# Optimization experiments

Measured on AMD Instinct MI355X. Metric: run time of the kernel, lower is better.

## Reference

```python
import jax, jax.numpy as jnp
import numpy as np

H = 8      # n_heads
HD = 64    # per-head channels (out_channels in __init__, before *= n_heads)


def setup_inputs() -> dict:
    key = jax.random.key(0)
    ks = jax.random.split(key, 10)
    B, C, N = 4, 256, 2048
    O = H * HD
    s = 1.0 / np.sqrt(C).astype(np.float32)
    return {
        "x": jax.random.normal(ks[0], (B, C, N), dtype=jnp.float32),
        "y": jax.random.normal(ks[1], (B, C, N), dtype=jnp.float32),
        "Wq": jax.random.normal(ks[2], (O, C), dtype=jnp.float32) * s,
        "bq": jnp.zeros((O,), dtype=jnp.float32),
        "Wk": jax.random.normal(ks[3], (O, C), dtype=jnp.float32) * s,
        "bk": jnp.zeros((O,), dtype=jnp.float32),
        "Wv": jax.random.normal(ks[4], (O, C), dtype=jnp.float32) * s,
        "bv": jnp.zeros((O,), dtype=jnp.float32),
        "Wp": jax.random.normal(ks[5], (HD, C), dtype=jnp.float32) * s,  # residual projection, bias=False
        "gamma": jax.random.uniform(ks[6], (H, 1, 1, 1), dtype=jnp.float32) + 0.001,
    }


def _conv1x1(W, b, t):
    # 1x1 Conv1d: (O,C) x (B,C,N) -> (B,O,N)
    out = jnp.einsum('oc,bcn->bon', W, t)
    return out if b is None else out + b[None, :, None]


def _heads(t):
    # (B, H*HD, N) -> (H, B, N, HD); channel split into contiguous per-head chunks
    B, _, N = t.shape
    return t.reshape(B, H, HD, N).transpose(1, 0, 3, 2)


def reference(x, y, Wq, bq, Wk, bk, Wv, bv, Wp, gamma):
    # q/k/v projections via 1x1 convs (kernel_size=1, 'stride_effective' padding => same length)
    q = _heads(_conv1x1(Wq, bq, x))   # (H,B,N,HD)
    k = _heads(_conv1x1(Wk, bk, y))   # (H,B,N,HD)
    v = _heads(_conv1x1(Wv, bv, y))   # (H,B,N,HD)

    # energy = bmm(Q, K^T); softmax over last dim (no mask)
    energy = jnp.einsum('hbnd,hbmd->hbnm', q, k)          # (H,B,N,N)
    attn = jax.nn.softmax(energy, axis=-1)

    # out = bmm(attention.transpose(-2,-1), V)  (note the transpose in the original)
    out = jnp.einsum('hbnm,hbnd->hbmd', attn, v)          # (H,B,N,HD)

    # gamma-weighted residual blend with projected y
    yp = _conv1x1(Wp, None, y).transpose(0, 2, 1)         # (B,N,HD)
    g = gamma.reshape(H, 1, 1, 1)
    out = (g * out + yp[None]) / (1.0 + g)                # (H,B,N,HD)
    return out
```

## Files before the change

### kernel.cpp

```cpp
#include <hip/hip_runtime.h>
#include <math.h>
#include <stdint.h>

#define B_DIM 4
#define C_DIM 256
#define N_DIM 2048
#define H_DIM 8
#define HD    64
#define HB    32
#define NTOK  (B_DIM * N_DIM)
#define LOG2E 1.44269504f

typedef __attribute__((ext_vector_type(8))) short bf16x8;
typedef __attribute__((ext_vector_type(4))) float f32x4;
typedef __attribute__((ext_vector_type(16))) float f32x16;
typedef __attribute__((ext_vector_type(4))) unsigned u32x4;

static __device__ __forceinline__ short f2bf(float f) {
    unsigned u = __builtin_bit_cast(unsigned, f);
    u += 0x7fffu + ((u >> 16) & 1u);
    return (short)(u >> 16);
}
static __device__ __forceinline__ float bf2f(short s) {
    unsigned u = ((unsigned)(unsigned short)s) << 16;
    return __builtin_bit_cast(float, u);
}
static __device__ __forceinline__ float fx2(float x) {
#if __has_builtin(__builtin_amdgcn_exp2f)
    return __builtin_amdgcn_exp2f(x);
#else
    return exp2f(x);
#endif
}
static __device__ __forceinline__ unsigned pk_bf16(float a, float b) {
#if __has_builtin(__builtin_amdgcn_cvt_pk_bf16_f32)
    auto v = __builtin_amdgcn_cvt_pk_bf16_f32(a, b);
    return __builtin_bit_cast(unsigned, v);
#else
    unsigned ua = __builtin_bit_cast(unsigned, a);
    unsigned ub = __builtin_bit_cast(unsigned, b);
    return ((ua + 0x8000u) >> 16) | ((ub + 0x8000u) & 0xffff0000u);
#endif
}
static __device__ __forceinline__ void pl32swap(unsigned &a, unsigned &b) {
#if __has_builtin(__builtin_amdgcn_permlane32_swap)
    typedef __attribute__((ext_vector_type(2))) int i32x2_t;
    i32x2_t r = __builtin_amdgcn_permlane32_swap((int)a, (int)b, false, false);
    a = (unsigned)r[0]; b = (unsigned)r[1];
#else
    unsigned sa = __shfl_xor(a, 32), sb = __shfl_xor(b, 32);
    bool hi = (threadIdx.x & 32) != 0;
    unsigned na = hi ? sb : a;
    unsigned nb = hi ? b : sa;
    a = na; b = nb;
#endif
}

static __device__ __forceinline__ void gll16(const void* g, void* ldsbase, int lane) {
#if __has_builtin(__builtin_amdgcn_global_load_lds)
    __builtin_amdgcn_global_load_lds(
        (const __attribute__((address_space(1))) void*)(uintptr_t)(g),
        (__attribute__((address_space(3))) void*)(uintptr_t)(ldsbase), 16, 0, 0);
#else
    *(bf16x8*)((char*)ldsbase + lane * 16) = *(const bf16x8*)g;
#endif
}

#define MFMA16(A, Bv, Cv) __builtin_amdgcn_mfma_f32_16x16x32_bf16(A, Bv, Cv, 0, 0, 0)
#define MFMA32(A, Bv, Cv) __builtin_amdgcn_mfma_f32_32x32x16_bf16(A, Bv, Cv, 0, 0, 0)


__global__ __launch_bounds__(256) void cast_all(
    const float* __restrict__ X, const float* __restrict__ Y,
    const float* __restrict__ Wq, const float* __restrict__ Wk,
    const float* __restrict__ Wv, const float* __restrict__ Wp,
    short* __restrict__ XS, short* __restrict__ YS,
    short* __restrict__ WSx, short* __restrict__ WSy)
{
    const int z = blockIdx.z;
    const int t = threadIdx.x;

    if (z == 8) {
        int base = (blockIdx.y * 32 + blockIdx.x) * 256 + t;
#pragma unroll
        for (int rep = 0; rep < 2; ++rep) {
            int gid = base + rep * 32768;
            if (gid >= 51200) break;
            int lane = gid & 63, chunk = gid >> 6;
            int lo = lane & 15, quad = lane >> 4;
            const float* src; short* dst;
            if (chunk < 256) {
                int ot = chunk >> 3, ks = chunk & 7;
                src = Wq + (size_t)(ot * 16 + lo) * C_DIM + ks * 32 + quad * 8;
                dst = WSx + (size_t)chunk * 512 + lane * 8;
            } else {
                int ch = chunk - 256;
                int ot = ch >> 3, ks = ch & 7;
                int row = ot * 16 + lo;
                const float* basep = (row < 512) ? (Wk + (size_t)row * C_DIM)
                                   : (row < 1024) ? (Wv + (size_t)(row - 512) * C_DIM)
                                                  : (Wp + (size_t)(row - 1024) * C_DIM);
                src = basep + ks * 32 + quad * 8;
                dst = WSy + (size_t)ch * 512 + lane * 8;
            }
            bf16x8 o;
#pragma unroll
            for (int j = 0; j < 8; ++j) o[j] = f2bf(src[j]);
            *(bf16x8*)dst = o;
        }
        return;
    }

    const float* src = (z < 4) ? X : Y;
    short* dst = (z < 4) ? XS : YS;
    const int b = z & 3, c0 = blockIdx.y * 64, n0 = blockIdx.x * 64;
    __shared__ float L[64][65];
    for (int i = t; i < 4096; i += 256) {
        int cc = i >> 6, nn = i & 63;
        L[cc][nn] = src[((size_t)b * C_DIM + c0 + cc) * N_DIM + n0 + nn];
    }
    __syncthreads();
#pragma unroll
    for (int half = 0; half < 2; ++half) {
        int cid = half * 256 + t;
        int lane = cid & 63, fi = cid >> 6;
        int ksl = fi & 1, rtl = fi >> 1;
        int lo = lane & 15, quad = lane >> 4;
        bf16x8 o;
#pragma unroll
        for (int j = 0; j < 8; ++j) o[j] = f2bf(L[ksl * 32 + quad * 8 + j][rtl * 16 + lo]);
        int rt = b * 128 + (n0 >> 4) + rtl;
        int ks = (c0 >> 5) + ksl;
        *(bf16x8*)(dst + ((size_t)(rt * 8 + ks) * 64 + lane) * 8) = o;
    }
}

__global__ __launch_bounds__(256) void proj_all(
    const short* __restrict__ WSx, const short* __restrict__ WSy,
    const short* __restrict__ XS, const short* __restrict__ YS,
    const float* __restrict__ bq, const float* __restrict__ bk,
    const float* __restrict__ bv,
    short* __restrict__ QS, short* __restrict__ KS,
    short* __restrict__ VSu, float* __restrict__ Yo)
{
    const int oy = blockIdx.y;
    const bool isq = oy < 8;
    const short* WS = isq ? WSx : WSy;
    const short* Xs = isq ? XS : YS;
    const int oyl = isq ? oy : oy - 8;
    const int o0 = oyl * 64;
    const int tok0 = blockIdx.x * 128;
    const int t = threadIdx.x, wave = t >> 6, lane = t & 63;
    const int lo = lane & 15, quad = lane >> 4;

    __shared__ __align__(16) char smem[34816];

    const int ot = oyl * 4 + wave;
    const int rt0 = tok0 >> 4;
    const f32x4 czero = {0.f, 0.f, 0.f, 0.f};

    f32x4 acc[8];
#pragma unroll
    for (int i = 0; i < 8; ++i) acc[i] = czero;

#pragma unroll 2
    for (int ks = 0; ks < 8; ++ks) {
        bf16x8 a = *(const bf16x8*)(WS + ((size_t)(ot * 8 + ks) * 64 + lane) * 8);
#pragma unroll
        for (int nt = 0; nt < 8; ++nt) {
            bf16x8 bx = *(const bf16x8*)(Xs + ((size_t)((rt0 + nt) * 8 + ks) * 64 + lane) * 8);
            acc[nt] = MFMA16(a, bx, acc[nt]);
        }
    }

    const int b = tok0 >> 11;
    const int n0b = tok0 & (N_DIM - 1);

    if (oy < 16) {
        short* T = (short*)smem;
        const float* bias = isq ? bq : bk;
        const float scale = isq ? LOG2E : 1.f;
        float bvr[4];
#pragma unroll
        for (int r = 0; r < 4; ++r) bvr[r] = bias[o0 + wave * 16 + quad * 4 + r];
#pragma unroll
        for (int nt = 0; nt < 8; ++nt) {
            short4 pk;
            pk.x = f2bf((acc[nt][0] + bvr[0]) * scale);
            pk.y = f2bf((acc[nt][1] + bvr[1]) * scale);
            pk.z = f2bf((acc[nt][2] + bvr[2]) * scale);
            pk.w = f2bf((acc[nt][3] + bvr[3]) * scale);
            *(short4*)(T + (nt * 16 + lo) * 72 + wave * 16 + quad * 4) = pk;
        }
        __syncthreads();
        const int h = oyl;
        const int hb = h * 4 + b;
        short* dst = isq ? QS : KS;
#pragma unroll
        for (int s = 0; s < 4; ++s) {
            int cid = s * 256 + t;
            int ln = cid & 63, fi = cid >> 6;
            int ks = fi & 3, nt2l = fi >> 2;
            bf16x8 v = *(const bf16x8*)(T + (nt2l * 32 + (ln & 31)) * 72
                                          + ks * 16 + ((ln >> 5) << 3));
            size_t frag = ((size_t)(hb * 64) + (n0b >> 5) + nt2l) * 4 + ks;
            *(bf16x8*)(dst + frag * 512 + ln * 8) = v;
        }
    } else if (oy < 24) {
        short* T2 = (short*)smem;
        float bvr[4];
#pragma unroll
        for (int r = 0; r < 4; ++r) bvr[r] = bv[o0 - 512 + wave * 16 + quad * 4 + r];
#pragma unroll
        for (int nt = 0; nt < 8; ++nt)
#pragma unroll
            for (int r = 0; r < 4; ++r) {
                int ol = wave * 16 + quad * 4 + r;
                T2[ol * 136 + nt * 16 + lo] = f2bf(acc[nt][r] + bvr[r]);
            }
        __syncthreads();
        const int h = oy - 16;
        const int hb = h * 4 + b;
#pragma unroll
        for (int s = 0; s < 4; ++s) {
            int cid = s * 256 + t;
            int ln = cid & 63, fi = cid >> 6;
            int dt2 = fi & 1, nk = (fi >> 1) & 3, nbl = fi >> 3;
            bf16x8 v = *(const bf16x8*)(T2 + (dt2 * 32 + (ln & 31)) * 136
                                           + nbl * 64 + nk * 16 + ((ln >> 5) << 3));
            size_t frag = (((size_t)(hb * 32) + (n0b >> 6) + nbl) * 4 + nk) * 2 + dt2;
            *(bf16x8*)(VSu + frag * 512 + ln * 8) = v;
        }
    } else {
        float* T3 = (float*)smem;
#pragma unroll
        for (int nt = 0; nt < 8; ++nt) {
            float4 f;
            f.x = acc[nt][0]; f.y = acc[nt][1]; f.z = acc[nt][2]; f.w = acc[nt][3];
            *(float4*)(T3 + (nt * 16 + lo) * 68 + wave * 16 + quad * 4) = f;
        }
        __syncthreads();
#pragma unroll
        for (int s = 0; s < 8; ++s) {
            int cid = s * 256 + t;
            int row = cid >> 4, c4 = (cid & 15) * 4;
            float4 f = *(const float4*)(T3 + row * 68 + c4);
            *(float4*)(Yo + ((size_t)(tok0 + row)) * 64 + c4) = f;
        }
    }
}

__global__ __launch_bounds__(256, 4) void rowsum_mfma(
    const short* __restrict__ QS, const short* __restrict__ KS,
    float* __restrict__ RSp, float* __restrict__ RSpW)
{
    const int id = blockIdx.x;
    const int hb = ((id & 7) << 2) | ((id >> 3) & 3);
    const int zq = (id >> 5) & 3;
    const int n0 = (id >> 7) * 256;
    const int t = threadIdx.x, wave = t >> 6, lane = t & 63;
    const int hi = lane >> 5;
    f32x16 czero16;
#pragma unroll
    for (int r = 0; r < 16; ++r) czero16[r] = 0.f;

    bf16x8 qf[2][4];
    const short* qb = QS + ((size_t)(hb * 64 + (n0 >> 5) + wave * 2)) * 4 * 512 + lane * 8;
#pragma unroll
    for (int tt = 0; tt < 2; ++tt)
#pragma unroll
        for (int ks = 0; ks < 4; ++ks)
            qf[tt][ks] = *(const bf16x8*)(qb + (tt * 4 + ks) * 512);

    float sm[2][16];
#pragma unroll
    for (int tt = 0; tt < 2; ++tt)
#pragma unroll
        for (int r = 0; r < 16; ++r) sm[tt][r] = 0.f;

    const short* kp = KS + ((size_t)(hb * 64 + zq * 16)) * 4 * 512 + lane * 8;
    for (int mt = 0; mt < 16; ++mt) {
        bf16x8 kf[4];
#pragma unroll
        for (int ks = 0; ks < 4; ++ks)
            kf[ks] = *(const bf16x8*)(kp + (mt * 4 + ks) * 512);
#pragma unroll
        for (int tt = 0; tt < 2; ++tt) {
            f32x16 cc = czero16;
#pragma unroll
            for (int ks = 0; ks < 4; ++ks) cc = MFMA32(qf[tt][ks], kf[ks], cc);
#pragma unroll
            for (int r = 0; r < 16; ++r) sm[tt][r] += fx2(cc[r]);
        }
    }

#pragma unroll
    for (int sft = 1; sft < 32; sft <<= 1)
#pragma unroll
        for (int tt = 0; tt < 2; ++tt)
#pragma unroll
            for (int r = 0; r < 16; ++r) sm[tt][r] += __shfl_xor(sm[tt][r], sft);

    if ((lane & 31) == 0) {
        float* dst = (zq < 2) ? (RSp  + (size_t)zq * HB * N_DIM)
                              : (RSpW + (size_t)(zq - 2) * HB * N_DIM);
#pragma unroll
        for (int tt = 0; tt < 2; ++tt)
#pragma unroll
            for (int g = 0; g < 4; ++g) {
                int n = n0 + wave * 64 + tt * 32 + g * 8 + hi * 4;
                float4 v = {sm[tt][g * 4 + 0], sm[tt][g * 4 + 1],
                            sm[tt][g * 4 + 2], sm[tt][g * 4 + 3]};
                *(float4*)(dst + (size_t)hb * N_DIM + n) = v;
            }
    }
}

__global__ __launch_bounds__(256) void v_scale(
    const short* __restrict__ VSu, const float* __restrict__ RSp,
    const float* __restrict__ RSpW, short* __restrict__ VS)
{
    int t = blockIdx.x * 256 + threadIdx.x;
    int lane = t & 63, fidx = t >> 6;
    int dt2 = fidx & 1; (void)dt2;
    int nk = (fidx >> 1) & 3, nb = (fidx >> 3) & 31, hb = fidx >> 8;
    int n = nb * 64 + nk * 16 + ((lane >> 5) << 3);
    bf16x8 v = *(const bf16x8*)(VSu + (size_t)t * 8);
    const float* r0 = RSp  + (size_t)hb * N_DIM + n;
    const float* r1 = r0 + (size_t)HB * N_DIM;
    const float* r2 = RSpW + (size_t)hb * N_DIM + n;
    const float* r3 = r2 + (size_t)HB * N_DIM;
    bf16x8 o;
#pragma unroll
    for (int j = 0; j < 8; ++j)
        o[j] = f2bf(bf2f(v[j]) / ((r0[j] + r1[j]) + (r2[j] + r3[j])));
    *(bf16x8*)(VS + (size_t)t * 8) = o;
}

__global__ __launch_bounds__(256, 3) void attnout_mfma(
    const short* __restrict__ QS, const short* __restrict__ KS,
    const short* __restrict__ VS,
    short* __restrict__ PA0, short* __restrict__ PA1)
{
    const int id = blockIdx.x;
    const int hb = ((id & 7) << 2) | ((id >> 3) & 3);
    const int z = (id >> 5) & 1;
    const int m0 = (id >> 6) * 128;

    __shared__ __align__(16) char smem[34816];
    char* Qst = smem;
    char* Vst = smem + 16384;

    const int t = threadIdx.x, wave = t >> 6, lane = t & 63;
    const f32x4 cz4 = {0.f, 0.f, 0.f, 0.f}; (void)cz4;
    f32x16 czero16;
#pragma unroll
    for (int r = 0; r < 16; ++r) czero16[r] = 0.f;

    bf16x8 kf[4];
    {
        const short* kbase = KS + ((size_t)(hb * 64 + (m0 >> 5) + wave)) * 4 * 512 + lane * 8;
#pragma unroll
        for (int ks = 0; ks < 4; ++ks)
            kf[ks] = *(const bf16x8*)(kbase + ks * 512);
    }

    f32x16 oacc[2];
#pragma unroll
    for (int dt2 = 0; dt2 < 2; ++dt2) oacc[dt2] = czero16;

    const short* qsrc = QS + ((size_t)(hb * 64 + z * 32)) * 4 * 512 + lane * 8;
    const short* vsrc = VS + ((size_t)(hb * 32 + z * 16)) * 8 * 512 + lane * 8;
    const int NIT = N_DIM / 2 / 64;

    f32x16 c[2];
    bf16x8 pa[4];

    gll16(qsrc + (size_t)wave * 512,            Qst + wave * 1024, lane);
    gll16(qsrc + (size_t)(wave + 4) * 512,      Qst + (wave + 4) * 1024, lane);
    gll16(qsrc + (size_t)(8 + wave) * 512,      Qst + 8192 + wave * 1024, lane);
    gll16(qsrc + (size_t)(8 + wave + 4) * 512,  Qst + 8192 + (wave + 4) * 1024, lane);
    gll16(vsrc + (size_t)wave * 512,            Vst + wave * 1024, lane);
    gll16(vsrc + (size_t)(wave + 4) * 512,      Vst + (wave + 4) * 1024, lane);
    __syncthreads();
#pragma unroll
    for (int tt = 0; tt < 2; ++tt) {
        f32x16 cc = czero16;
#pragma unroll
        for (int ks = 0; ks < 4; ++ks) {
            bf16x8 a = *(const bf16x8*)(Qst + (tt * 4 + ks) * 1024 + lane * 16);
            cc = MFMA32(a, kf[ks], cc);
        }
        c[tt] = cc;
    }
    __syncthreads();

    for (int i = 0; i < NIT - 1; ++i) {
        gll16(qsrc + ((size_t)(i + 2) * 8 + wave) * 512,
              Qst + (i & 1) * 8192 + wave * 1024, lane);
        gll16(qsrc + ((size_t)(i + 2) * 8 + wave + 4) * 512,
              Qst + (i & 1) * 8192 + (wave + 4) * 1024, lane);
        gll16(vsrc + ((size_t)(i + 1) * 8 + wave) * 512,
              Vst + ((i + 1) & 1) * 8192 + wave * 1024, lane);
        gll16(vsrc + ((size_t)(i + 1) * 8 + wave + 4) * 512,
              Vst + ((i + 1) & 1) * 8192 + (wave + 4) * 1024, lane);
#pragma unroll
        for (int tt = 0; tt < 2; ++tt) {
#pragma unroll
            for (int half = 0; half < 2; ++half) {
                unsigned w01 = pk_bf16(fx2(c[tt][half * 8 + 0]), fx2(c[tt][half * 8 + 1]));
                unsigned w23 = pk_bf16(fx2(c[tt][half * 8 + 2]), fx2(c[tt][half * 8 + 3]));
                unsigned w45 = pk_bf16(fx2(c[tt][half * 8 + 4]), fx2(c[tt][half * 8 + 5]));
                unsigned w67 = pk_bf16(fx2(c[tt][half * 8 + 6]), fx2(c[tt][half * 8 + 7]));
                pl32swap(w01, w45);
                pl32swap(w23, w67);
                u32x4 f = {w01, w23, w45, w67};
                pa[tt * 2 + half] = __builtin_bit_cast(bf16x8, f);
            }
        }
        {
            const char* Qb = Qst + ((i + 1) & 1) * 8192;
            __builtin_amdgcn_s_setprio(1);
#pragma unroll
            for (int tt = 0; tt < 2; ++tt) {
                f32x16 cc = czero16;
#pragma unroll
                for (int ks = 0; ks < 4; ++ks) {
                    bf16x8 a = *(const bf16x8*)(Qb + (tt * 4 + ks) * 1024 + lane * 16);
                    cc = MFMA32(a, kf[ks], cc);
                }
                c[tt] = cc;
            }
            __builtin_amdgcn_s_setprio(0);
        }
        {
            const char* vb = Vst + (i & 1) * 8192;
#pragma unroll
            for (int nk = 0; nk < 4; ++nk)
#pragma unroll
                for (int dt2 = 0; dt2 < 2; ++dt2) {
                    bf16x8 bv = *(const bf16x8*)(vb + (nk * 2 + dt2) * 1024 + lane * 16);
                    oacc[dt2] = MFMA32(pa[nk], bv, oacc[dt2]);
                }
        }
        __syncthreads();
    }

#pragma unroll
    for (int tt = 0; tt < 2; ++tt) {
#pragma unroll
        for (int half = 0; half < 2; ++half) {
            unsigned w01 = pk_bf16(fx2(c[tt][half * 8 + 0]), fx2(c[tt][half * 8 + 1]));
            unsigned w23 = pk_bf16(fx2(c[tt][half * 8 + 2]), fx2(c[tt][half * 8 + 3]));
            unsigned w45 = pk_bf16(fx2(c[tt][half * 8 + 4]), fx2(c[tt][half * 8 + 5]));
            unsigned w67 = pk_bf16(fx2(c[tt][half * 8 + 6]), fx2(c[tt][half * 8 + 7]));
            pl32swap(w01, w45);
            pl32swap(w23, w67);
            u32x4 f = {w01, w23, w45, w67};
            pa[tt * 2 + half] = __builtin_bit_cast(bf16x8, f);
        }
    }
    {
        const char* vb = Vst + ((NIT - 1) & 1) * 8192;
#pragma unroll
        for (int nk = 0; nk < 4; ++nk)
#pragma unroll
            for (int dt2 = 0; dt2 < 2; ++dt2) {
                bf16x8 bv = *(const bf16x8*)(vb + (nk * 2 + dt2) * 1024 + lane * 16);
                oacc[dt2] = MFMA32(pa[nk], bv, oacc[dt2]);
            }
    }

    short* PA = z ? PA1 : PA0;
    float* T = (float*)smem;
    const int hi = lane >> 5;
    __syncthreads();
#pragma unroll
    for (int dt2 = 0; dt2 < 2; ++dt2)
#pragma unroll
        for (int r = 0; r < 16; ++r) {
            int row = wave * 32 + (r & 3) + 8 * (r >> 2) + 4 * hi;
            T[row * 68 + dt2 * 32 + (lane & 31)] = oacc[dt2][r];
        }
    __syncthreads();
#pragma unroll
    for (int it = 0; it < 4; ++it) {
        int idx = it * 256 + t;
        int rowl = idx >> 3, dg = (idx & 7) * 8;
        float4 f0 = *(const float4*)(T + rowl * 68 + dg);
        float4 f1 = *(const float4*)(T + rowl * 68 + dg + 4);
        uint4 o;
        o.x = pk_bf16(f0.x, f0.y);
        o.y = pk_bf16(f0.z, f0.w);
        o.z = pk_bf16(f1.x, f1.y);
        o.w = pk_bf16(f1.z, f1.w);
        int m = m0 + rowl;
        *(uint4*)(PA + ((size_t)(hb * N_DIM + m)) * 64 + dg) = o;
    }
}

__global__ __launch_bounds__(256) void combine_out(
    const short* __restrict__ PA0, const short* __restrict__ PA1,
    const float* __restrict__ YP, const float* __restrict__ gamma,
    float* __restrict__ out)
{
    size_t flat = ((size_t)blockIdx.x * 256 + threadIdx.x) * 8;
    int d  = (int)(flat & 63);
    int n  = (int)((flat >> 6) & (N_DIM - 1));
    int hb = (int)(flat >> 17);
    int h = hb >> 2, b = hb & 3;
    float g = gamma[h];
    float inv = 1.f / (1.f + g);
    float gi = g * inv;
    bf16x8 p0 = *(const bf16x8*)(PA0 + flat);
    bf16x8 p1 = *(const bf16x8*)(PA1 + flat);
    const float* yp = YP + ((size_t)b * N_DIM + n) * HD + d;
    float o[8];
#pragma unroll
    for (int j = 0; j < 8; ++j)
        o[j] = gi * (bf2f(p0[j]) + bf2f(p1[j])) + inv * yp[j];
    float4 o0 = {o[0], o[1], o[2], o[3]};
    float4 o1 = {o[4], o[5], o[6], o[7]};
    *(float4*)(out + flat) = o0;
    *(float4*)(out + flat + 4) = o1;
}

extern "C" void kernel_launch(void* const* d_in, const int* in_sizes, int n_in,
                              void* d_out, int out_size, void* d_ws, size_t ws_size,
                              hipStream_t stream) {
    const float* x     = (const float*)d_in[0];
    const float* y     = (const float*)d_in[1];
    const float* Wq    = (const float*)d_in[2];
    const float* bq    = (const float*)d_in[3];
    const float* Wk    = (const float*)d_in[4];
    const float* bk    = (const float*)d_in[5];
    const float* Wv    = (const float*)d_in[6];
    const float* bv    = (const float*)d_in[7];
    const float* Wp    = (const float*)d_in[8];
    const float* gamma = (const float*)d_in[9];
    float* out = (float*)d_out;

    const size_t XEL  = (size_t)B_DIM * C_DIM * N_DIM;
    const size_t QKV  = (size_t)HB * N_DIM * HD;

    short* XS  = (short*)d_ws;
    short* YS  = XS + XEL;
    short* WSx = YS + XEL;
    short* WSy = WSx + 512 * C_DIM;
    short* QS  = WSy + 1088 * C_DIM;
    short* KS  = QS + QKV;
    short* VSu = KS + QKV;
    short* VS  = VSu + QKV;
    float* YPb = (float*)(VS + QKV);
    float* RSp = YPb + (size_t)B_DIM * N_DIM * HD;
    short* PA0 = XS;
    short* PA1 = VSu;
    float* RSpW = (float*)WSx;

    dim3 blk(256);
    cast_all<<<dim3(N_DIM / 64, C_DIM / 64, 9), blk, 0, stream>>>(
        x, y, Wq, Wk, Wv, Wp, XS, YS, WSx, WSy);

    proj_all<<<dim3(NTOK / 128, 25), blk, 0, stream>>>(
        WSx, WSy, XS, YS, bq, bk, bv, QS, KS, VSu, YPb);

    rowsum_mfma<<<dim3(1024), blk, 0, stream>>>(QS, KS, RSp, RSpW);
    v_scale<<<dim3(2048), blk, 0, stream>>>(VSu, RSp, RSpW, VS);
    attnout_mfma<<<dim3(1024), blk, 0, stream>>>(QS, KS, VS, PA0, PA1);
    combine_out<<<dim3(2048), blk, 0, stream>>>(PA0, PA1, YPb, gamma, out);
}
```

Baseline: 191.9 us.

## Process two m-tiles per block in attnout to reuse staged Q and V

Each attnout block now covers 256 output rows instead of 128. Every wave holds two sets of K fragments and two output accumulators, so each Q and V tile staged in shared memory feeds twice as many MFMAs. This halves the block count and the global and LDS traffic for Q and V per unit of work. In exchange, register pressure rises, launch bounds drop to 2 blocks per CU, and the grid shrinks to 512 blocks, which may hurt latency hiding or leave CUs underfilled.

```diff
diff --git a/kernel.cpp b/kernel.cpp
--- a/kernel.cpp
+++ b/kernel.cpp
@@ -337,7 +337,7 @@
     *(bf16x8*)(VS + (size_t)t * 8) = o;
 }
 
-__global__ __launch_bounds__(256, 3) void attnout_mfma(
+__global__ __launch_bounds__(256, 2) void attnout_mfma(
     const short* __restrict__ QS, const short* __restrict__ KS,
     const short* __restrict__ VS,
     short* __restrict__ PA0, short* __restrict__ PA1)
@@ -345,36 +345,39 @@
     const int id = blockIdx.x;
     const int hb = ((id & 7) << 2) | ((id >> 3) & 3);
     const int z = (id >> 5) & 1;
-    const int m0 = (id >> 6) * 128;
+    const int m0 = (id >> 6) * 256;
 
     __shared__ __align__(16) char smem[34816];
     char* Qst = smem;
     char* Vst = smem + 16384;
 
     const int t = threadIdx.x, wave = t >> 6, lane = t & 63;
-    const f32x4 cz4 = {0.f, 0.f, 0.f, 0.f}; (void)cz4;
     f32x16 czero16;
 #pragma unroll
     for (int r = 0; r < 16; ++r) czero16[r] = 0.f;
 
-    bf16x8 kf[4];
-    {
-        const short* kbase = KS + ((size_t)(hb * 64 + (m0 >> 5) + wave)) * 4 * 512 + lane * 8;
+    bf16x8 kf[2][4];
+#pragma unroll
+    for (int mm = 0; mm < 2; ++mm) {
+        const short* kbase = KS + ((size_t)(hb * 64 + (m0 >> 5) + mm * 4 + wave)) * 4 * 512
+                           + lane * 8;
 #pragma unroll
         for (int ks = 0; ks < 4; ++ks)
-            kf[ks] = *(const bf16x8*)(kbase + ks * 512);
-    }
-
-    f32x16 oacc[2];
-#pragma unroll
-    for (int dt2 = 0; dt2 < 2; ++dt2) oacc[dt2] = czero16;
+            kf[mm][ks] = *(const bf16x8*)(kbase + ks * 512);
+    }
+
+    f32x16 oacc[2][2];
+#pragma unroll
+    for (int mm = 0; mm < 2; ++mm)
+#pragma unroll
+        for (int dt2 = 0; dt2 < 2; ++dt2) oacc[mm][dt2] = czero16;
 
     const short* qsrc = QS + ((size_t)(hb * 64 + z * 32)) * 4 * 512 + lane * 8;
     const short* vsrc = VS + ((size_t)(hb * 32 + z * 16)) * 8 * 512 + lane * 8;
     const int NIT = N_DIM / 2 / 64;
 
-    f32x16 c[2];
-    bf16x8 pa[4];
+    f32x16 c[2][2];
+    bf16x8 pa[2][4];
 
     gll16(qsrc + (size_t)wave * 512,            Qst + wave * 1024, lane);
     gll16(qsrc + (size_t)(wave + 4) * 512,      Qst + (wave + 4) * 1024, lane);
@@ -385,13 +388,14 @@
     __syncthreads();
 #pragma unroll
     for (int tt = 0; tt < 2; ++tt) {
-        f32x16 cc = czero16;
+        f32x16 c0 = czero16, c1 = czero16;
 #pragma unroll
         for (int ks = 0; ks < 4; ++ks) {
             bf16x8 a = *(const bf16x8*)(Qst + (tt * 4 + ks) * 1024 + lane * 16);
-            cc = MFMA32(a, kf[ks], cc);
-        }
-        c[tt] = cc;
+            c0 = MFMA32(a, kf[0][ks], c0);
+            c1 = MFMA32(a, kf[1][ks], c1);
+        }
+        c[tt][0] = c0; c[tt][1] = c1;
     }
     __syncthreads();
 
@@ -405,61 +409,65 @@
         gll16(vsrc + ((size_t)(i + 1) * 8 + wave + 4) * 512,
               Vst + ((i + 1) & 1) * 8192 + (wave + 4) * 1024, lane);
 #pragma unroll
-        for (int tt = 0; tt < 2; ++tt) {
+        for (int mm = 0; mm < 2; ++mm)
+#pragma unroll
+            for (int tt = 0; tt < 2; ++tt)
+#pragma unroll
+                for (int half = 0; half < 2; ++half) {
+                    unsigned w01 = pk_bf16(fx2(c[tt][mm][half * 8 + 0]), fx2(c[tt][mm][half * 8 + 1]));
+                    unsigned w23 = pk_bf16(fx2(c[tt][mm][half * 8 + 2]), fx2(c[tt][mm][half * 8 + 3]));
+                    unsigned w45 = pk_bf16(fx2(c[tt][mm][half * 8 + 4]), fx2(c[tt][mm][half * 8 + 5]));
+                    unsigned w67 = pk_bf16(fx2(c[tt][mm][half * 8 + 6]), fx2(c[tt][mm][half * 8 + 7]));
+                    pl32swap(w01, w45);
+                    pl32swap(w23, w67);
+                    u32x4 f = {w01, w23, w45, w67};
+                    pa[mm][tt * 2 + half] = __builtin_bit_cast(bf16x8, f);
+                }
+        {
+            const char* Qb = Qst + ((i + 1) & 1) * 8192;
+            __builtin_amdgcn_s_setprio(1);
+#pragma unroll
+            for (int tt = 0; tt < 2; ++tt) {
+                f32x16 c0 = czero16, c1 = czero16;
+#pragma unroll
+                for (int ks = 0; ks < 4; ++ks) {
+                    bf16x8 a = *(const bf16x8*)(Qb + (tt * 4 + ks) * 1024 + lane * 16);
+                    c0 = MFMA32(a, kf[0][ks], c0);
+                    c1 = MFMA32(a, kf[1][ks], c1);
+                }
+                c[tt][0] = c0; c[tt][1] = c1;
+            }
+            __builtin_amdgcn_s_setprio(0);
+        }
+        {
+            const char* vb = Vst + (i & 1) * 8192;
+#pragma unroll
+            for (int nk = 0; nk < 4; ++nk)
+#pragma unroll
+                for (int dt2 = 0; dt2 < 2; ++dt2) {
+                    bf16x8 bv = *(const bf16x8*)(vb + (nk * 2 + dt2) * 1024 + lane * 16);
+                    oacc[0][dt2] = MFMA32(pa[0][nk], bv, oacc[0][dt2]);
+                    oacc[1][dt2] = MFMA32(pa[1][nk], bv, oacc[1][dt2]);
+                }
+        }
+        __syncthreads();
+    }
+
+#pragma unroll
+    for (int mm = 0; mm < 2; ++mm)
+#pragma unroll
+        for (int tt = 0; tt < 2; ++tt)
 #pragma unroll
             for (int half = 0; half < 2; ++half) {
-                unsigned w01 = pk_bf16(fx2(c[tt][half * 8 + 0]), fx2(c[tt][half * 8 + 1]));
-                unsigned w23 = pk_bf16(fx2(c[tt][half * 8 + 2]), fx2(c[tt][half * 8 + 3]));
-                unsigned w45 = pk_bf16(fx2(c[tt][half * 8 + 4]), fx2(c[tt][half * 8 + 5]));
-                unsigned w67 = pk_bf16(fx2(c[tt][half * 8 + 6]), fx2(c[tt][half * 8 + 7]));
+                unsigned w01 = pk_bf16(fx2(c[tt][mm][half * 8 + 0]), fx2(c[tt][mm][half * 8 + 1]));
+                unsigned w23 = pk_bf16(fx2(c[tt][mm][half * 8 + 2]), fx2(c[tt][mm][half * 8 + 3]));
+                unsigned w45 = pk_bf16(fx2(c[tt][mm][half * 8 + 4]), fx2(c[tt][mm][half * 8 + 5]));
+                unsigned w67 = pk_bf16(fx2(c[tt][mm][half * 8 + 6]), fx2(c[tt][mm][half * 8 + 7]));
                 pl32swap(w01, w45);
                 pl32swap(w23, w67);
                 u32x4 f = {w01, w23, w45, w67};
-                pa[tt * 2 + half] = __builtin_bit_cast(bf16x8, f);
-            }
-        }
-        {
-            const char* Qb = Qst + ((i + 1) & 1) * 8192;
-            __builtin_amdgcn_s_setprio(1);
-#pragma unroll
-            for (int tt = 0; tt < 2; ++tt) {
-                f32x16 cc = czero16;
-#pragma unroll
-                for (int ks = 0; ks < 4; ++ks) {
-                    bf16x8 a = *(const bf16x8*)(Qb + (tt * 4 + ks) * 1024 + lane * 16);
-                    cc = MFMA32(a, kf[ks], cc);
-                }
-                c[tt] = cc;
-            }
-            __builtin_amdgcn_s_setprio(0);
-        }
-        {
-            const char* vb = Vst + (i & 1) * 8192;
-#pragma unroll
-            for (int nk = 0; nk < 4; ++nk)
-#pragma unroll
-                for (int dt2 = 0; dt2 < 2; ++dt2) {
-                    bf16x8 bv = *(const bf16x8*)(vb + (nk * 2 + dt2) * 1024 + lane * 16);
-                    oacc[dt2] = MFMA32(pa[nk], bv, oacc[dt2]);
-                }
-        }
-        __syncthreads();
-    }
-
-#pragma unroll
-    for (int tt = 0; tt < 2; ++tt) {
-#pragma unroll
-        for (int half = 0; half < 2; ++half) {
-            unsigned w01 = pk_bf16(fx2(c[tt][half * 8 + 0]), fx2(c[tt][half * 8 + 1]));
-            unsigned w23 = pk_bf16(fx2(c[tt][half * 8 + 2]), fx2(c[tt][half * 8 + 3]));
-            unsigned w45 = pk_bf16(fx2(c[tt][half * 8 + 4]), fx2(c[tt][half * 8 + 5]));
-            unsigned w67 = pk_bf16(fx2(c[tt][half * 8 + 6]), fx2(c[tt][half * 8 + 7]));
-            pl32swap(w01, w45);
-            pl32swap(w23, w67);
-            u32x4 f = {w01, w23, w45, w67};
-            pa[tt * 2 + half] = __builtin_bit_cast(bf16x8, f);
-        }
-    }
+                pa[mm][tt * 2 + half] = __builtin_bit_cast(bf16x8, f);
+            }
     {
         const char* vb = Vst + ((NIT - 1) & 1) * 8192;
 #pragma unroll
@@ -467,35 +475,39 @@
 #pragma unroll
             for (int dt2 = 0; dt2 < 2; ++dt2) {
                 bf16x8 bv = *(const bf16x8*)(vb + (nk * 2 + dt2) * 1024 + lane * 16);
-                oacc[dt2] = MFMA32(pa[nk], bv, oacc[dt2]);
+                oacc[0][dt2] = MFMA32(pa[0][nk], bv, oacc[0][dt2]);
+                oacc[1][dt2] = MFMA32(pa[1][nk], bv, oacc[1][dt2]);
             }
     }
 
     short* PA = z ? PA1 : PA0;
     float* T = (float*)smem;
     const int hi = lane >> 5;
-    __syncthreads();
-#pragma unroll
-    for (int dt2 = 0; dt2 < 2; ++dt2)
-#pragma unroll
-        for (int r = 0; r < 16; ++r) {
-            int row = wave * 32 + (r & 3) + 8 * (r >> 2) + 4 * hi;
-            T[row * 68 + dt2 * 32 + (lane & 31)] = oacc[dt2][r];
-        }
-    __syncthreads();
-#pragma unroll
-    for (int it = 0; it < 4; ++it) {
-        int idx = it * 256 + t;
-        int rowl = idx >> 3, dg = (idx & 7) * 8;
-        float4 f0 = *(const float4*)(T + rowl * 68 + dg);
-        float4 f1 = *(const float4*)(T + rowl * 68 + dg + 4);
-        uint4 o;
-        o.x = pk_bf16(f0.x, f0.y);
-        o.y = pk_bf16(f0.z, f0.w);
-        o.z = pk_bf16(f1.x, f1.y);
-        o.w = pk_bf16(f1.z, f1.w);
-        int m = m0 + rowl;
-        *(uint4*)(PA + ((size_t)(hb * N_DIM + m)) * 64 + dg) = o;
+#pragma unroll
+    for (int mm = 0; mm < 2; ++mm) {
+        __syncthreads();
+#pragma unroll
+        for (int dt2 = 0; dt2 < 2; ++dt2)
+#pragma unroll
+            for (int r = 0; r < 16; ++r) {
+                int row = wave * 32 + (r & 3) + 8 * (r >> 2) + 4 * hi;
+                T[row * 68 + dt2 * 32 + (lane & 31)] = oacc[mm][dt2][r];
+            }
+        __syncthreads();
+#pragma unroll
+        for (int it = 0; it < 4; ++it) {
+            int idx = it * 256 + t;
+            int rowl = idx >> 3, dg = (idx & 7) * 8;
+            float4 f0 = *(const float4*)(T + rowl * 68 + dg);
+            float4 f1 = *(const float4*)(T + rowl * 68 + dg + 4);
+            uint4 o;
+            o.x = pk_bf16(f0.x, f0.y);
+            o.y = pk_bf16(f0.z, f0.w);
+            o.z = pk_bf16(f1.x, f1.y);
+            o.w = pk_bf16(f1.z, f1.w);
+            int m = m0 + mm * 128 + rowl;
+            *(uint4*)(PA + ((size_t)(hb * N_DIM + m)) * 64 + dg) = o;
+        }
     }
 }
 
@@ -566,6 +578,6 @@
 
     rowsum_mfma<<<dim3(1024), blk, 0, stream>>>(QS, KS, RSp, RSpW);
     v_scale<<<dim3(2048), blk, 0, stream>>>(VSu, RSp, RSpW, VS);
-    attnout_mfma<<<dim3(1024), blk, 0, stream>>>(QS, KS, VS, PA0, PA1);
+    attnout_mfma<<<dim3(512), blk, 0, stream>>>(QS, KS, VS, PA0, PA1);
     combine_out<<<dim3(2048), blk, 0, stream>>>(PA0, PA1, YPb, gamma, out);
 }
```

Result: no change. 189.0 us (-1.5%).
